# Optimization experiments

Hardware: AMD Instinct MI355X
Metric: run time of the kernel (lower is better)

Reference implementation:

```python
import jax, jax.numpy as jnp
import numpy as np
from jax import lax

DN = ('NHWC', 'HWIO', 'NHWC')


def _conv(x, w, b=None, stride=1):
    y = lax.conv_general_dilated(x, w, (stride, stride), 'SAME', dimension_numbers=DN)
    return y + b if b is not None else y


def _conv_t(x, w, b, stride=2):
    y = lax.conv_transpose(x, w, (stride, stride), 'SAME', dimension_numbers=DN)
    return y + b


def _res_stack(x, blocks):
    # ResidualBlock: x + Conv1x1(relu(Conv3x3(relu(x)))); final relu after stack
    for w1, w2 in blocks:
        t = jax.nn.relu(x)
        t = _conv(t, w1)          # 3x3, no bias
        t = jax.nn.relu(t)
        t = _conv(t, w2)          # 1x1, no bias
        x = x + t
    return jax.nn.relu(x)


def setup_inputs() -> dict:
    key = jax.random.key(0)
    ks = jax.random.split(key, 32)
    s = 0.05
    n = lambda i, shape: jax.random.normal(ks[i], shape, dtype=jnp.float32) * s
    H, RH, D, K = 128, 32, 128, 512
    return {
        'x': jax.random.normal(ks[0], (16, 256, 256, 3), dtype=jnp.float32),
        'emb': jax.random.normal(ks[1], (K, D), dtype=jnp.float32),  # stddev 1.0 init
        'enc_w1': n(2, (4, 4, 3, H // 2)),  'enc_b1': jnp.zeros((H // 2,), jnp.float32),
        'enc_w2': n(3, (4, 4, H // 2, H)),  'enc_b2': jnp.zeros((H,), jnp.float32),
        'enc_w3': n(4, (3, 3, H, H)),       'enc_b3': jnp.zeros((H,), jnp.float32),
        'erb1_w1': n(5, (3, 3, H, RH)), 'erb1_w2': n(6, (1, 1, RH, H)),
        'erb2_w1': n(7, (3, 3, H, RH)), 'erb2_w2': n(8, (1, 1, RH, H)),
        'dec_w': n(9, (3, 3, D, H)),        'dec_b': jnp.zeros((H,), jnp.float32),
        'drb1_w1': n(10, (3, 3, H, RH)), 'drb1_w2': n(11, (1, 1, RH, H)),
        'drb2_w1': n(12, (3, 3, H, RH)), 'drb2_w2': n(13, (1, 1, RH, H)),
        'dt1_w': n(14, (4, 4, H, H // 2)),  'dt1_b': jnp.zeros((H // 2,), jnp.float32),
        'dt2_w': n(15, (4, 4, H // 2, 3)),  'dt2_b': jnp.zeros((3,), jnp.float32),
    }


def _forward(x, emb, enc_w1, enc_b1, enc_w2, enc_b2, enc_w3, enc_b3,
             erb1_w1, erb1_w2, erb2_w1, erb2_w2,
             dec_w, dec_b, drb1_w1, drb1_w2, drb2_w1, drb2_w2,
             dt1_w, dt1_b, dt2_w, dt2_b):
    f = jax.nn.relu(_conv(x, enc_w1, enc_b1, 2))
    f = jax.nn.relu(_conv(f, enc_w2, enc_b2, 2))
    f = _conv(f, enc_w3, enc_b3, 1)
    f = _res_stack(f, [(erb1_w1, erb1_w2), (erb2_w1, erb2_w2)])
    # VQ: full [N, K] squared-distance matrix, argmin, codebook gather
    D = emb.shape[1]
    flat = f.reshape(-1, D)                                   # [N, D]
    dist = ((flat ** 2).sum(axis=1, keepdims=True)
            + (emb ** 2).sum(axis=1)[None, :]
            - 2.0 * flat @ emb.T)                              # [N, K]
    idx = jnp.argmin(dist, axis=1)                             # [N]
    q = emb[idx].reshape(f.shape)                              # quantized
    y = _conv(q, dec_w, dec_b, 1)
    y = _res_stack(y, [(drb1_w1, drb1_w2), (drb2_w1, drb2_w2)])
    y = jax.nn.relu(_conv_t(y, dt1_w, dt1_b))
    y = _conv_t(y, dt2_w, dt2_b)
    return (y, f, q)


def reference(x, emb, enc_w1, enc_b1, enc_w2, enc_b2, enc_w3, enc_b3,
              erb1_w1, erb1_w2, erb2_w1, erb2_w2,
              dec_w, dec_b, drb1_w1, drb1_w2, drb2_w1, drb2_w2,
              dt1_w, dt1_b, dt2_w, dt2_b):
    return _forward(x, emb, enc_w1, enc_b1, enc_w2, enc_b2, enc_w3, enc_b3,
                    erb1_w1, erb1_w2, erb2_w1, erb2_w2,
                    dec_w, dec_b, drb1_w1, drb1_w2, drb2_w1, drb2_w2,
                    dt1_w, dt1_b, dt2_w, dt2_b)
```

## Files before the change

### kernel.cpp

```cpp
#include <hip/hip_runtime.h>
#include <hip/hip_bf16.h>
#include <hip/hip_fp16.h>

using bf16 = __hip_bfloat16;
using frag_ab = __attribute__((ext_vector_type(8))) short;
using f16x8  = __attribute__((ext_vector_type(8))) _Float16;
using frag_cd = __attribute__((ext_vector_type(4))) float;

enum { F_INRELU = 1, F_OUTRELU = 2, F_RES = 4 };

struct TapSet { int dy[16]; int dx[16]; int wi[16]; };

__device__ __forceinline__ unsigned int relu_pk(unsigned int v) {
    unsigned int m = ((v & 0x80008000u) >> 15) * 0xFFFFu;
    return v & ~m;
}
__device__ __forceinline__ unsigned int mask_by(unsigned int v, unsigned int h) {
    unsigned int m = ((h & 0x80008000u) >> 15) * 0xFFFFu;
    return v & ~m;
}
__device__ __forceinline__ int xcd_swz(int bx, int n) {
    return (bx & 7) * (n >> 3) + (bx >> 3);
}

__global__ void pack_w_k(const float* __restrict__ w, bf16* __restrict__ dst,
                         int Ci, int Co, int BN, TapSet taps, int total)
{
    int idx = blockIdx.x * 256 + threadIdx.x;
    if (idx >= total) return;
    int j  = idx & 7;
    int r1 = idx >> 3;
    int nl = r1 % BN;
    int r2 = r1 / BN;
    int q  = r2 & 3;
    int cb = r2 >> 2;
    int nblocks = Co / BN;
    int c  = cb / nblocks;
    int nb = cb - c * nblocks;
    int cpt = Ci >> 5;
    int tap = c / cpt;
    int ci  = (c - tap * cpt) * 32 + q * 8 + j;
    int n   = nb * BN + nl;
    dst[idx] = __float2bfloat16(w[(size_t)(taps.wi[tap] * Ci + ci) * Co + n]);
}

__global__ void pack_w2_k(const float* __restrict__ w, __half* __restrict__ dst,
                          int Ci, int Co, int BN, TapSet taps, int total)
{
    int idx = blockIdx.x * 256 + threadIdx.x;
    if (idx >= total) return;
    int j  = idx & 7;
    int r1 = idx >> 3;
    int nl = r1 % BN;
    int r2 = r1 / BN;
    int q  = r2 & 3;
    int cb = r2 >> 2;
    int nblocks = Co / BN;
    int c  = cb / nblocks;
    int nb = cb - c * nblocks;
    int cpt = Ci >> 5;
    int tap = c / cpt;
    int ci  = (c - tap * cpt) * 32 + q * 8 + j;
    int n   = nb * BN + nl;
    float v = w[(size_t)(taps.wi[tap] * Ci + ci) * Co + n];
    __half h = __float2half(v);
    __half l = __float2half((v - __half2float(h)) * 2048.0f);
    size_t base = (size_t)cb * (BN * 64) + (q * BN + nl) * 8 + j;
    dst[base] = h;
    dst[base + BN * 32] = l;
}

__global__ void pack_wdt2_k(const float* __restrict__ w, __half* __restrict__ dst)
{
    int idx = blockIdx.x * 256 + threadIdx.x;
    if (idx >= 16384) return;
    int parity = idx >> 12;
    int r0 = idx & 4095;
    int j  = r0 & 7;
    int r1 = r0 >> 3;
    int nl = r1 & 15;
    int r2 = r1 >> 4;
    int q  = r2 & 3;
    int cb = r2 >> 2;
    int tap = cb >> 1;
    int cc  = cb & 1;
    int ci  = cc * 32 + q * 8 + j;
    int n   = nl;
    int py = parity >> 1, px = parity & 1;
    int ty = tap >> 1, tx = tap & 1;
    int wi = (py + 2 * ty) * 4 + (px + 2 * tx);
    float v = (n < 3) ? w[(size_t)(wi * 64 + ci) * 3 + n] : 0.f;
    __half h = __float2half(v);
    __half l = __float2half((v - __half2float(h)) * 2048.0f);
    size_t base = (size_t)parity * 8192 + cb * 1024 + (q * 16 + nl) * 8 + j;
    dst[base] = h;
    dst[base + 512] = l;
}

__global__ void pack_we1_k(const float* __restrict__ w, __half* __restrict__ dst)
{
    int idx = blockIdx.x * 256 + threadIdx.x;
    if (idx >= 4096) return;
    int j  = idx & 7;
    int r1 = idx >> 3;
    int nl = r1 & 63;
    int r2 = r1 >> 6;
    int q  = r2 & 3;
    int c  = r2 >> 2;
    int k  = c * 32 + q * 8 + j;
    int tap = k >> 2, ci = k & 3;
    float v = (ci < 3) ? w[(size_t)(tap * 3 + ci) * 64 + nl] : 0.f;
    __half h = __float2half(v);
    __half l = __float2half((v - __half2float(h)) * 2048.0f);
    size_t base = (size_t)c * 4096 + (q * 64 + nl) * 8 + j;
    dst[base] = h;
    dst[base + 2048] = l;
}

__global__ __launch_bounds__(256) void pad_x_k(
    const float* __restrict__ x, __half* __restrict__ xh, __half* __restrict__ xl)
{
    int pix = blockIdx.x * 256 + threadIdx.x;
    const float* ip = x + (size_t)pix * 3;
    float v0 = ip[0], v1 = ip[1], v2 = ip[2];
    unsigned short hb[4], lb[4];
    float vv[4] = {v0, v1, v2, 0.f};
#pragma unroll
    for (int i = 0; i < 4; ++i) {
        __half h = __float2half(vv[i]);
        hb[i] = __half_as_ushort(h);
        lb[i] = __half_as_ushort(__float2half((vv[i] - __half2float(h)) * 2048.0f));
    }
    uint2 hv = make_uint2((unsigned)hb[0] | ((unsigned)hb[1] << 16),
                          (unsigned)hb[2] | ((unsigned)hb[3] << 16));
    uint2 lv = make_uint2((unsigned)lb[0] | ((unsigned)lb[1] << 16),
                          (unsigned)lb[2] | ((unsigned)lb[3] << 16));
    *(uint2*)(xh + (size_t)pix * 4) = hv;
    *(uint2*)(xl + (size_t)pix * 4) = lv;
}

__global__ __launch_bounds__(256) void enc1_mfma_k(
    const __half* __restrict__ xh, const __half* __restrict__ xl,
    const __half* __restrict__ wp, const float* __restrict__ bias,
    __half* __restrict__ oh, __half* __restrict__ ol)
{
    __shared__ __align__(16) short Ash[64 * 32];
    __shared__ __align__(16) short Asl[64 * 32];
    __shared__ __align__(16) short Bsh[64 * 32];
    __shared__ __align__(16) short Bsl[64 * 32];

    const int tid = threadIdx.x;
    const int m0 = xcd_swz(blockIdx.x, 4096) * 64;

    const int am = tid >> 2;
    const int aq = tid & 3;
    const int gm  = m0 + am;
    const int nn_ = gm >> 14;
    const int rr_ = gm & 16383;
    const int iy0 = (rr_ >> 7) * 2 - 1;
    const int ix0 = (rr_ & 127) * 2 - 1;

    const int lane = tid & 63;
    const int wv4 = tid >> 6;
    const int wm = (wv4 & 1) * 32;
    const int wn = (wv4 >> 1) * 32;
    const int lm = lane & 15, lq = lane >> 4;

    frag_cd accA[2][2], accB[2][2];
#pragma unroll
    for (int i = 0; i < 2; ++i)
#pragma unroll
        for (int j = 0; j < 2; ++j)
#pragma unroll
            for (int r = 0; r < 4; ++r) { accA[i][j][r] = 0.f; accB[i][j][r] = 0.f; }

#pragma unroll
    for (int c = 0; c < 2; ++c) {
        const int tap = c * 8 + aq * 2;
        const int ky = tap >> 2, kx = tap & 3;
        const int iy = iy0 + ky;
        const int ix = ix0 + kx;
        uint2 h0 = make_uint2(0u, 0u), h1 = h0, l0 = h0, l1 = h0;
        if (iy >= 0 && iy < 256) {
            const size_t rowb = (size_t)(nn_ * 256 + iy) * 256;
            if (ix >= 0 && ix < 256) {
                h0 = *(const uint2*)(xh + (rowb + ix) * 4);
                l0 = *(const uint2*)(xl + (rowb + ix) * 4);
            }
            if (ix + 1 >= 0 && ix + 1 < 256) {
                h1 = *(const uint2*)(xh + (rowb + ix + 1) * 4);
                l1 = *(const uint2*)(xl + (rowb + ix + 1) * 4);
            }
        }
        __syncthreads();
        *(uint4*)&Ash[(aq * 64 + am) * 8] = make_uint4(h0.x, h0.y, h1.x, h1.y);
        *(uint4*)&Asl[(aq * 64 + am) * 8] = make_uint4(l0.x, l0.y, l1.x, l1.y);
        {
            const __half* wc = wp + (size_t)c * 4096;
            *(uint4*)&Bsh[tid * 8] = *(const uint4*)(wc + tid * 8);
            *(uint4*)&Bsl[tid * 8] = *(const uint4*)(wc + 2048 + tid * 8);
        }
        __syncthreads();

        f16x8 afh[2], afl[2], bfh[2], bfl[2];
#pragma unroll
        for (int i = 0; i < 2; ++i) {
            afh[i] = *(const f16x8*)&Ash[(lq * 64 + wm + i * 16 + lm) * 8];
            afl[i] = *(const f16x8*)&Asl[(lq * 64 + wm + i * 16 + lm) * 8];
        }
#pragma unroll
        for (int j = 0; j < 2; ++j) {
            bfh[j] = *(const f16x8*)&Bsh[(lq * 64 + wn + j * 16 + lm) * 8];
            bfl[j] = *(const f16x8*)&Bsl[(lq * 64 + wn + j * 16 + lm) * 8];
        }
#pragma unroll
        for (int i = 0; i < 2; ++i)
#pragma unroll
            for (int j = 0; j < 2; ++j) {
                accA[i][j] = __builtin_amdgcn_mfma_f32_16x16x32_f16(afh[i], bfh[j], accA[i][j], 0, 0, 0);
                accB[i][j] = __builtin_amdgcn_mfma_f32_16x16x32_f16(afh[i], bfl[j], accB[i][j], 0, 0, 0);
                accB[i][j] = __builtin_amdgcn_mfma_f32_16x16x32_f16(afl[i], bfh[j], accB[i][j], 0, 0, 0);
            }
    }

    const float s = 1.0f / 2048.0f;
#pragma unroll
    for (int j = 0; j < 2; ++j) {
        const int n_g = wn + j * 16 + lm;
        const float bv = bias[n_g];
#pragma unroll
        for (int i = 0; i < 2; ++i) {
#pragma unroll
            for (int r = 0; r < 4; ++r) {
                const int m_g = m0 + wm + i * 16 + lq * 4 + r;
                const size_t ob = (size_t)m_g * 64 + n_g;
                float v = accA[i][j][r] + accB[i][j][r] * s + bv;
                v = fmaxf(v, 0.f);
                __half h = __float2half(v);
                oh[ob] = h;
                ol[ob] = __float2half((v - __half2float(h)) * 2048.0f);
            }
        }
    }
}

template<int BN>
__global__ __launch_bounds__(256) void conv_mfma2_k(
    const __half* __restrict__ ah, const __half* __restrict__ al,
    const __half* __restrict__ wp, const float* __restrict__ bias,
    float* __restrict__ out, __half* __restrict__ oh, __half* __restrict__ ol,
    const __half* __restrict__ rh, const __half* __restrict__ rl,
    int IH, int IW, int Ci, int Co, int sy_in,
    TapSet taps, int ntaps, int flags)
{
    __shared__ __align__(16) short Ash[64 * 32];
    __shared__ __align__(16) short Asl[64 * 32];
    __shared__ __align__(16) short Bsh[BN * 32];
    __shared__ __align__(16) short Bsl[BN * 32];

    const int tid = threadIdx.x;
    const int m0 = xcd_swz(blockIdx.x, gridDim.x) * 64;
    const int n0 = blockIdx.y * BN;

    const int am = tid >> 2;
    const int aq = tid & 3;
    const int gm  = m0 + am;
    const int nn_ = gm >> 12;
    const int rr_ = gm & 4095;
    const int oy_ = (rr_ >> 6) * sy_in;
    const int ox_ = (rr_ & 63) * sy_in;

    const int lane = tid & 63;
    const int wv4 = tid >> 6;
    constexpr int MT = (BN >= 64) ? 2 : 1;
    constexpr int NT = (BN == 128) ? 4 : 2;
    const int wm = (BN >= 64) ? (wv4 & 1) * 32 : wv4 * 16;
    const int wn = (BN == 128) ? (wv4 >> 1) * 64 : ((BN == 64) ? (wv4 >> 1) * 32 : 0);
    const int lm = lane & 15, lq = lane >> 4;
    constexpr int NLOAD = BN * 32 / 8;

    frag_cd accA[MT][NT], accB[MT][NT];
#pragma unroll
    for (int i = 0; i < MT; ++i)
#pragma unroll
        for (int j = 0; j < NT; ++j)
#pragma unroll
            for (int r = 0; r < 4; ++r) { accA[i][j][r] = 0.f; accB[i][j][r] = 0.f; }

    const int cpt = Ci >> 5;
    const int nch = ntaps * cpt;
    const bool inrelu = (flags & F_INRELU) != 0;

    int tap = 0, cc = 0, ci0 = 0;
    for (int c = 0; c < nch; ++c) {
        const int iy = oy_ + taps.dy[tap];
        const int ix = ox_ + taps.dx[tap];
        uint4 avh = make_uint4(0u, 0u, 0u, 0u);
        uint4 avl = make_uint4(0u, 0u, 0u, 0u);
        if (iy >= 0 && iy < IH && ix >= 0 && ix < IW) {
            const size_t off = (size_t)((nn_ * IH + iy) * IW + ix) * Ci + ci0 + aq * 8;
            avh = *(const uint4*)(ah + off);
            avl = *(const uint4*)(al + off);
        }
        if (inrelu) {
            avl.x = mask_by(avl.x, avh.x); avl.y = mask_by(avl.y, avh.y);
            avl.z = mask_by(avl.z, avh.z); avl.w = mask_by(avl.w, avh.w);
            avh.x = relu_pk(avh.x); avh.y = relu_pk(avh.y);
            avh.z = relu_pk(avh.z); avh.w = relu_pk(avh.w);
        }
        uint4 bvh0, bvl0, bvh1, bvl1;
        {
            const __half* wc = wp + (size_t)(c * gridDim.y + blockIdx.y) * (BN * 64);
            if constexpr (BN == 128) {
                bvh0 = *(const uint4*)(wc + tid * 8);
                bvh1 = *(const uint4*)(wc + (256 + tid) * 8);
                bvl0 = *(const uint4*)(wc + BN * 32 + tid * 8);
                bvl1 = *(const uint4*)(wc + BN * 32 + (256 + tid) * 8);
            } else if (tid < NLOAD) {
                bvh0 = *(const uint4*)(wc + tid * 8);
                bvl0 = *(const uint4*)(wc + BN * 32 + tid * 8);
            }
        }

        __syncthreads();
        *(uint4*)&Ash[(aq * 64 + am) * 8] = avh;
        *(uint4*)&Asl[(aq * 64 + am) * 8] = avl;
        if constexpr (BN == 128) {
            *(uint4*)&Bsh[tid * 8] = bvh0;
            *(uint4*)&Bsh[(256 + tid) * 8] = bvh1;
            *(uint4*)&Bsl[tid * 8] = bvl0;
            *(uint4*)&Bsl[(256 + tid) * 8] = bvl1;
        } else if (tid < NLOAD) {
            *(uint4*)&Bsh[tid * 8] = bvh0;
            *(uint4*)&Bsl[tid * 8] = bvl0;
        }
        __syncthreads();

        f16x8 afh[MT], afl[MT], bfh[NT], bfl[NT];
#pragma unroll
        for (int i = 0; i < MT; ++i) {
            afh[i] = *(const f16x8*)&Ash[(lq * 64 + wm + i * 16 + lm) * 8];
            afl[i] = *(const f16x8*)&Asl[(lq * 64 + wm + i * 16 + lm) * 8];
        }
#pragma unroll
        for (int j = 0; j < NT; ++j) {
            bfh[j] = *(const f16x8*)&Bsh[(lq * BN + wn + j * 16 + lm) * 8];
            bfl[j] = *(const f16x8*)&Bsl[(lq * BN + wn + j * 16 + lm) * 8];
        }
#pragma unroll
        for (int i = 0; i < MT; ++i)
#pragma unroll
            for (int j = 0; j < NT; ++j) {
                accA[i][j] = __builtin_amdgcn_mfma_f32_16x16x32_f16(afh[i], bfh[j], accA[i][j], 0, 0, 0);
                accB[i][j] = __builtin_amdgcn_mfma_f32_16x16x32_f16(afh[i], bfl[j], accB[i][j], 0, 0, 0);
                accB[i][j] = __builtin_amdgcn_mfma_f32_16x16x32_f16(afl[i], bfh[j], accB[i][j], 0, 0, 0);
            }

        ci0 += 32;
        if (++cc == cpt) { cc = 0; ci0 = 0; ++tap; }
    }

    const float s = 1.0f / 2048.0f;
#pragma unroll
    for (int j = 0; j < NT; ++j) {
        const int n_g = n0 + wn + j * 16 + lm;
        const float bv = bias ? bias[n_g] : 0.f;
#pragma unroll
        for (int i = 0; i < MT; ++i) {
#pragma unroll
            for (int r = 0; r < 4; ++r) {
                const int m_g = m0 + wm + i * 16 + lq * 4 + r;
                const size_t ob = (size_t)m_g * Co + n_g;
                float v = accA[i][j][r] + accB[i][j][r] * s + bv;
                if (flags & F_RES)
                    v += __half2float(rh[ob]) + __half2float(rl[ob]) * s;
                if (flags & F_OUTRELU) v = fmaxf(v, 0.f);
                if (out) out[ob] = v;
                if (oh) {
                    __half h = __float2half(v);
                    oh[ob] = h;
                    ol[ob] = __float2half((v - __half2float(h)) * 2048.0f);
                }
            }
        }
    }
}

template<int BN>
__global__ __launch_bounds__(256) void conv_mfma_k(
    const bf16* __restrict__ a, const bf16* __restrict__ wp,
    const float* __restrict__ bias,
    float* __restrict__ out, bf16* __restrict__ out_bf,
    const float* __restrict__ res,
    int Ci, int Co, int OHf, int OWf, int sy_out, int py, int px,
    TapSet taps, int ntaps, int flags)
{
    __shared__ __align__(16) short As[64 * 32];
    __shared__ __align__(16) short Bs[BN * 32];

    const int tid = threadIdx.x;
    const int m0 = xcd_swz(blockIdx.x, gridDim.x) * 64;
    const int n0 = blockIdx.y * BN;

    const int am = tid >> 2;
    const int aq = tid & 3;
    const int gm  = m0 + am;
    const int nn_ = gm >> 12;
    const int rr_ = gm & 4095;
    const int oy_ = rr_ >> 6;
    const int ox_ = rr_ & 63;

    const int lane = tid & 63;
    const int wv4 = tid >> 6;
    constexpr int MT = (BN >= 64) ? 2 : 1;
    constexpr int NT = (BN == 128) ? 4 : 2;
    const int wm = (BN >= 64) ? (wv4 & 1) * 32 : wv4 * 16;
    const int wn = (BN == 128) ? (wv4 >> 1) * 64 : ((BN == 64) ? (wv4 >> 1) * 32 : 0);
    const int lm = lane & 15, lq = lane >> 4;
    constexpr int NLOAD = BN * 32 / 8;

    frag_cd acc[MT][NT];
#pragma unroll
    for (int i = 0; i < MT; ++i)
#pragma unroll
        for (int j = 0; j < NT; ++j)
#pragma unroll
            for (int r = 0; r < 4; ++r) acc[i][j][r] = 0.f;

    const int cpt = Ci >> 5;
    const int nch = ntaps * cpt;
    const bool inrelu = (flags & F_INRELU) != 0;

    int tap = 0, cc = 0, ci0 = 0;
    for (int c = 0; c < nch; ++c) {
        const int iy = oy_ + taps.dy[tap];
        const int ix = ox_ + taps.dx[tap];
        uint4 av = make_uint4(0u, 0u, 0u, 0u);
        if (iy >= 0 && iy < 64 && ix >= 0 && ix < 64)
            av = *(const uint4*)(a + (size_t)((nn_ * 64 + iy) * 64 + ix) * Ci + ci0 + aq * 8);
        if (inrelu) {
            av.x = relu_pk(av.x); av.y = relu_pk(av.y);
            av.z = relu_pk(av.z); av.w = relu_pk(av.w);
        }
        uint4 bv0, bv1;
        {
            const bf16* wc = wp + ((size_t)c * gridDim.y + blockIdx.y) * (BN * 32);
            if constexpr (BN == 128) {
                bv0 = *(const uint4*)(wc + tid * 8);
                bv1 = *(const uint4*)(wc + (256 + tid) * 8);
            } else if (tid < NLOAD) {
                bv0 = *(const uint4*)(wc + tid * 8);
            }
        }

        __syncthreads();
        *(uint4*)&As[(aq * 64 + am) * 8] = av;
        if constexpr (BN == 128) {
            *(uint4*)&Bs[tid * 8] = bv0;
            *(uint4*)&Bs[(256 + tid) * 8] = bv1;
        } else if (tid < NLOAD) {
            *(uint4*)&Bs[tid * 8] = bv0;
        }
        __syncthreads();

        frag_ab af[MT], bfr[NT];
#pragma unroll
        for (int i = 0; i < MT; ++i)
            af[i] = *(const frag_ab*)&As[(lq * 64 + wm + i * 16 + lm) * 8];
#pragma unroll
        for (int j = 0; j < NT; ++j)
            bfr[j] = *(const frag_ab*)&Bs[(lq * BN + wn + j * 16 + lm) * 8];
#pragma unroll
        for (int i = 0; i < MT; ++i)
#pragma unroll
            for (int j = 0; j < NT; ++j)
                acc[i][j] = __builtin_amdgcn_mfma_f32_16x16x32_bf16(af[i], bfr[j], acc[i][j], 0, 0, 0);

        ci0 += 32;
        if (++cc == cpt) { cc = 0; ci0 = 0; ++tap; }
    }

#pragma unroll
    for (int j = 0; j < NT; ++j) {
        const int n_g = n0 + wn + j * 16 + lm;
        const float bv = bias ? bias[n_g] : 0.f;
#pragma unroll
        for (int i = 0; i < MT; ++i) {
#pragma unroll
            for (int r = 0; r < 4; ++r) {
                const int m_g = m0 + wm + i * 16 + lq * 4 + r;
                const int nn2 = m_g >> 12;
                const int rr2 = m_g & 4095;
                const int oy = (rr2 >> 6) * sy_out + py;
                const int ox = (rr2 & 63) * sy_out + px;
                const size_t ob = ((size_t)(nn2 * OHf + oy) * OWf + ox) * Co + n_g;
                float v = acc[i][j][r] + bv;
                if (flags & F_RES)     v += res[ob];
                if (flags & F_OUTRELU) v = fmaxf(v, 0.f);
                if (out)    out[ob]    = v;
                if (out_bf) out_bf[ob] = __float2bfloat16(v);
            }
        }
    }
}

__global__ __launch_bounds__(256) void dt2_mfma_k(
    const float* __restrict__ in,
    const __half* __restrict__ wp,
    const float* __restrict__ bias,
    float* __restrict__ out)
{
    __shared__ __align__(16) short Ash[64 * 32];
    __shared__ __align__(16) short Asl[64 * 32];
    __shared__ __align__(16) short Bsh[16 * 32];
    __shared__ __align__(16) short Bsl[16 * 32];

    const int tid = threadIdx.x;
    const int bx  = xcd_swz(blockIdx.x, 16384);
    const int par = bx & 3;
    const int m0  = (bx >> 2) * 64;
    const int py = par >> 1, px = par & 1;

    const int am = tid >> 2;
    const int aq = tid & 3;
    const int gm  = m0 + am;
    const int nn_ = gm >> 14;
    const int rr_ = gm & 16383;
    const int r_  = rr_ >> 7;
    const int c_  = rr_ & 127;

    const int lane = tid & 63;
    const int wv4 = tid >> 6;
    const int wm = wv4 * 16;
    const int lm = lane & 15, lq = lane >> 4;

    frag_cd accA, accB;
#pragma unroll
    for (int r = 0; r < 4; ++r) { accA[r] = 0.f; accB[r] = 0.f; }

    const __half* wpar = wp + (size_t)par * 8192;

    for (int c = 0; c < 8; ++c) {
        const int tap = c >> 1;
        const int iy = r_ + py + (tap >> 1) - 1;
        const int ix = c_ + px + (tap & 1) - 1;
        const int ci0 = (c & 1) * 32;
        uint4 hi = make_uint4(0u, 0u, 0u, 0u);
        uint4 lo = make_uint4(0u, 0u, 0u, 0u);
        if ((unsigned)iy < 128u && (unsigned)ix < 128u) {
            const float* ip = in + (size_t)((nn_ * 128 + iy) * 128 + ix) * 64 + ci0 + aq * 8;
            const float4 v0 = *(const float4*)ip;
            const float4 v1 = *(const float4*)(ip + 4);
            float vv[8] = {v0.x, v0.y, v0.z, v0.w, v1.x, v1.y, v1.z, v1.w};
            unsigned short hb[8], lb[8];
#pragma unroll
            for (int i = 0; i < 8; ++i) {
                __half h = __float2half(vv[i]);
                hb[i] = __half_as_ushort(h);
                lb[i] = __half_as_ushort(__float2half((vv[i] - __half2float(h)) * 2048.0f));
            }
            hi = make_uint4((unsigned)hb[0] | ((unsigned)hb[1] << 16),
                            (unsigned)hb[2] | ((unsigned)hb[3] << 16),
                            (unsigned)hb[4] | ((unsigned)hb[5] << 16),
                            (unsigned)hb[6] | ((unsigned)hb[7] << 16));
            lo = make_uint4((unsigned)lb[0] | ((unsigned)lb[1] << 16),
                            (unsigned)lb[2] | ((unsigned)lb[3] << 16),
                            (unsigned)lb[4] | ((unsigned)lb[5] << 16),
                            (unsigned)lb[6] | ((unsigned)lb[7] << 16));
        }
        uint4 bvh, bvl;
        if (tid < 64) {
            const __half* wc = wpar + c * 1024;
            bvh = *(const uint4*)(wc + tid * 8);
            bvl = *(const uint4*)(wc + 512 + tid * 8);
        }

        __syncthreads();
        *(uint4*)&Ash[(aq * 64 + am) * 8] = hi;
        *(uint4*)&Asl[(aq * 64 + am) * 8] = lo;
        if (tid < 64) {
            *(uint4*)&Bsh[tid * 8] = bvh;
            *(uint4*)&Bsl[tid * 8] = bvl;
        }
        __syncthreads();

        const f16x8 afh = *(const f16x8*)&Ash[(lq * 64 + wm + lm) * 8];
        const f16x8 afl = *(const f16x8*)&Asl[(lq * 64 + wm + lm) * 8];
        const f16x8 bfh = *(const f16x8*)&Bsh[(lq * 16 + lm) * 8];
        const f16x8 bfl = *(const f16x8*)&Bsl[(lq * 16 + lm) * 8];
        accA = __builtin_amdgcn_mfma_f32_16x16x32_f16(afh, bfh, accA, 0, 0, 0);
        accB = __builtin_amdgcn_mfma_f32_16x16x32_f16(afh, bfl, accB, 0, 0, 0);
        accB = __builtin_amdgcn_mfma_f32_16x16x32_f16(afl, bfh, accB, 0, 0, 0);
    }

    const float s = 1.0f / 2048.0f;
    if (lm < 3) {
        const float bv = bias[lm];
#pragma unroll
        for (int r = 0; r < 4; ++r) {
            const int m_g = m0 + wm + lq * 4 + r;
            const int nn2 = m_g >> 14;
            const int rr2 = m_g & 16383;
            const int oy = (rr2 >> 7) * 2 + py;
            const int ox = (rr2 & 127) * 2 + px;
            out[((size_t)(nn2 * 256 + oy) * 256 + ox) * 3 + lm] = accA[r] + accB[r] * s + bv;
        }
    }
}

__global__ void enorm_k(const float* __restrict__ emb, float* __restrict__ en) {
    int k = blockIdx.x * 256 + threadIdx.x;
    if (k >= 512) return;
    const float4* e = (const float4*)(emb + k * 128);
    float s = 0.f;
    for (int i = 0; i < 32; ++i) {
        float4 v = e[i];
        s += v.x * v.x + v.y * v.y + v.z * v.z + v.w * v.w;
    }
    en[k] = s;
}

__global__ void pack_emb_k(const float* __restrict__ emb, __half* __restrict__ dst)
{
    int idx = blockIdx.x * 256 + threadIdx.x;
    int k = idx & 127;
    int n = idx >> 7;
    float v = emb[idx];
    __half h = __float2half(v);
    __half l = __float2half((v - __half2float(h)) * 2048.0f);
    int nb = n >> 6, nl = n & 63;
    int ch = k >> 5, q = (k >> 3) & 3, j = k & 7;
    size_t base = (size_t)(nb * 4 + ch) * 4096 + (q * 64 + nl) * 8 + j;
    dst[base] = h;
    dst[base + 2048] = l;
}

__global__ __launch_bounds__(256) void vq_mfma_k(
    const __half* __restrict__ fh, const __half* __restrict__ fl,
    const __half* __restrict__ pe, const float* __restrict__ en,
    const float* __restrict__ emb, float* __restrict__ q, bf16* __restrict__ qb)
{
    __shared__ __align__(16) short Ash[64 * 128];
    __shared__ __align__(16) short Asl[64 * 128];
    __shared__ int sel[64];

    const int tid  = threadIdx.x;
    const int pos0 = blockIdx.x * 64;

    {
        const int am = tid >> 2;
        const int aq = tid & 3;
#pragma unroll
        for (int ch = 0; ch < 4; ++ch) {
            const size_t off = (size_t)(pos0 + am) * 128 + ch * 32 + aq * 8;
            uint4 vh = *(const uint4*)(fh + off);
            uint4 vl = *(const uint4*)(fl + off);
            *(uint4*)&Ash[((ch * 4 + aq) * 64 + am) * 8] = vh;
            *(uint4*)&Asl[((ch * 4 + aq) * 64 + am) * 8] = vl;
        }
    }
    __syncthreads();

    const int lane = tid & 63;
    const int w    = tid >> 6;
    const int lm = lane & 15, lq = lane >> 4;
    const int mbase = w * 16;
    const float s = 1.0f / 2048.0f;

    float best[4] = {3.4e38f, 3.4e38f, 3.4e38f, 3.4e38f};
    int   bidx[4] = {0, 0, 0, 0};

    f16x8 ah[4], alv[4];
#pragma unroll
    for (int ch = 0; ch < 4; ++ch) {
        ah[ch]  = *(const f16x8*)&Ash[((ch * 4 + lq) * 64 + mbase + lm) * 8];
        alv[ch] = *(const f16x8*)&Asl[((ch * 4 + lq) * 64 + mbase + lm) * 8];
    }

    for (int nb = 0; nb < 8; ++nb) {
        frag_cd accA[4], accB[4];
#pragma unroll
        for (int j = 0; j < 4; ++j)
#pragma unroll
            for (int r = 0; r < 4; ++r) { accA[j][r] = 0.f; accB[j][r] = 0.f; }

#pragma unroll
        for (int ch = 0; ch < 4; ++ch) {
            const __half* base = pe + (size_t)(nb * 4 + ch) * 4096;
            f16x8 bh[4], bl[4];
#pragma unroll
            for (int j = 0; j < 4; ++j) {
                const int o = (lq * 64 + j * 16 + lm) * 8;
                bh[j] = *(const f16x8*)(base + o);
                bl[j] = *(const f16x8*)(base + 2048 + o);
            }
#pragma unroll
            for (int j = 0; j < 4; ++j) {
                accA[j] = __builtin_amdgcn_mfma_f32_16x16x32_f16(ah[ch], bh[j], accA[j], 0, 0, 0);
                accB[j] = __builtin_amdgcn_mfma_f32_16x16x32_f16(ah[ch], bl[j], accB[j], 0, 0, 0);
                accB[j] = __builtin_amdgcn_mfma_f32_16x16x32_f16(alv[ch], bh[j], accB[j], 0, 0, 0);
            }
        }

#pragma unroll
        for (int j = 0; j < 4; ++j) {
            const int code = nb * 64 + j * 16 + lm;
            const float ec = en[code];
#pragma unroll
            for (int r = 0; r < 4; ++r) {
                float dot = accA[j][r] + accB[j][r] * s;
                float d = fmaf(dot, -2.f, ec);
                if (d < best[r]) { best[r] = d; bidx[r] = code; }
            }
        }
    }

#pragma unroll
    for (int r = 0; r < 4; ++r) {
        float d = best[r]; int ix = bidx[r];
#pragma unroll
        for (int m = 1; m < 16; m <<= 1) {
            float d2 = __shfl_xor(d, m);
            int   x2 = __shfl_xor(ix, m);
            if (d2 < d || (d2 == d && x2 < ix)) { d = d2; ix = x2; }
        }
        if (lm == 0) sel[mbase + lq * 4 + r] = ix;
    }
    __syncthreads();

#pragma unroll
    for (int jj = 0; jj < 32; ++jj) {
        int id = jj * 256 + tid;
        int p = id >> 7, k = id & 127;
        float v = emb[(size_t)sel[p] * 128 + k];
        q[(size_t)(pos0 + p) * 128 + k]  = v;
        qb[(size_t)(pos0 + p) * 128 + k] = __float2bfloat16(v);
    }
}

static TapSet conv_taps(int KH, int KW, int pad) {
    TapSet t{};
    for (int ky = 0; ky < KH; ++ky)
        for (int kx = 0; kx < KW; ++kx) {
            int i = ky * KW + kx;
            t.dy[i] = ky - pad; t.dx[i] = kx - pad; t.wi[i] = i;
        }
    return t;
}

static TapSet convt_taps(int py, int px) {
    TapSet t{};
    for (int ty = 0; ty < 2; ++ty)
        for (int tx = 0; tx < 2; ++tx) {
            int i = ty * 2 + tx;
            t.dy[i] = py + ty - 1;
            t.dx[i] = px + tx - 1;
            t.wi[i] = (py + 2 * ty) * 4 + (px + 2 * tx);
        }
    return t;
}

extern "C" void kernel_launch(void* const* d_in, const int* in_sizes, int n_in,
                              void* d_out, int out_size, void* d_ws, size_t ws_size,
                              hipStream_t stream)
{
    const float* x       = (const float*)d_in[0];
    const float* emb     = (const float*)d_in[1];
    const float* enc_w1  = (const float*)d_in[2];
    const float* enc_b1  = (const float*)d_in[3];
    const float* enc_w2  = (const float*)d_in[4];
    const float* enc_b2  = (const float*)d_in[5];
    const float* enc_w3  = (const float*)d_in[6];
    const float* enc_b3  = (const float*)d_in[7];
    const float* erb1_w1 = (const float*)d_in[8];
    const float* erb1_w2 = (const float*)d_in[9];
    const float* erb2_w1 = (const float*)d_in[10];
    const float* erb2_w2 = (const float*)d_in[11];
    const float* dec_w   = (const float*)d_in[12];
    const float* dec_b   = (const float*)d_in[13];
    const float* drb1_w1 = (const float*)d_in[14];
    const float* drb1_w2 = (const float*)d_in[15];
    const float* drb2_w1 = (const float*)d_in[16];
    const float* drb2_w2 = (const float*)d_in[17];
    const float* dt1_w   = (const float*)d_in[18];
    const float* dt1_b   = (const float*)d_in[19];
    const float* dt2_w   = (const float*)d_in[20];
    const float* dt2_b   = (const float*)d_in[21];

    char* wsb = (char*)d_ws;
    __half* H1 = (__half*)wsb;
    __half* L1 = (__half*)(wsb + (size_t)33554432);
    __half* H2 = (__half*)(wsb + (size_t)67108864);
    __half* L2 = (__half*)(wsb + (size_t)83886080);
    __half* Xh = (__half*)(wsb + (size_t)67108864);
    __half* Xl = (__half*)(wsb + (size_t)75497472);
    __half* H3 = (__half*)wsb;
    __half* L3 = (__half*)(wsb + (size_t)16777216);
    __half* H4 = (__half*)(wsb + (size_t)33554432);
    __half* L4 = (__half*)(wsb + (size_t)50331648);
    __half* Ht = (__half*)(wsb + (size_t)100663296);
    __half* Lt = (__half*)(wsb + (size_t)104857600);
    float*  EN = (float*)(wsb + (size_t)109051904);
    __half* Fh = (__half*)wsb;
    __half* Fl = (__half*)(wsb + (size_t)16777216);
    bf16* Qb  = (bf16*)(wsb + (size_t)67108864);
    bf16* Db  = (bf16*)(wsb + (size_t)83886080);
    bf16* Y1b = Qb;
    bf16* Y2b = Db;
    bf16* Tb  = (bf16*)(wsb + (size_t)100663296);
    float* Y0 = (float*)wsb;
    float* Y1 = (float*)(wsb + (size_t)33554432);
    float* A1 = (float*)wsb;
    char* pk = wsb + (size_t)109056000;
    bf16* Pdec  = (bf16*)pk;  pk += 147456 * 2;
    bf16* Pd1w1 = (bf16*)pk;  pk += 36864 * 2;
    bf16* Pd1w2 = (bf16*)pk;  pk += 4096 * 2;
    bf16* Pd2w1 = (bf16*)pk;  pk += 36864 * 2;
    bf16* Pd2w2 = (bf16*)pk;  pk += 4096 * 2;
    bf16* Pdt1[4];
    for (int i = 0; i < 4; ++i) { Pdt1[i] = (bf16*)pk; pk += 65536 * 2; }
    __half* P2enc2 = (__half*)pk; pk += 131072 * 4;
    __half* P2enc3 = (__half*)pk; pk += 147456 * 4;
    __half* P2e1w1 = (__half*)pk; pk += 36864 * 4;
    __half* P2e1w2 = (__half*)pk; pk += 4096 * 4;
    __half* P2e2w1 = (__half*)pk; pk += 36864 * 4;
    __half* P2e2w2 = (__half*)pk; pk += 4096 * 4;
    __half* Pe     = (__half*)pk; pk += 131072 * 2;
    __half* Pe1    = (__half*)pk; pk += 8192 * 2;
    __half* Pdt2   = (__half*)pk; pk += 32768 * 2;

    float* outY = (float*)d_out;
    float* outF = outY + 3145728;
    float* outQ = outF + 8388608;

    const TapSet t3 = conv_taps(3, 3, 1);
    const TapSet t4 = conv_taps(4, 4, 1);
    const TapSet t1 = conv_taps(1, 1, 0);
    TapSet tdt[4];
    for (int p = 0; p < 4; ++p) tdt[p] = convt_taps(p >> 1, p & 1);

    enorm_k<<<2, 256, 0, stream>>>(emb, EN);
    pack_emb_k<<<256, 256, 0, stream>>>(emb, Pe);
    pack_we1_k<<<16, 256, 0, stream>>>(enc_w1, Pe1);
    pack_wdt2_k<<<64, 256, 0, stream>>>(dt2_w, Pdt2);

    pack_w_k<<<(147456 + 255) / 256, 256, 0, stream>>>(dec_w, Pdec, 128, 128, 128, t3, 147456);
    pack_w_k<<<(36864 + 255) / 256, 256, 0, stream>>>(drb1_w1, Pd1w1, 128, 32, 32, t3, 36864);
    pack_w_k<<<(4096 + 255) / 256, 256, 0, stream>>>(drb1_w2, Pd1w2, 32, 128, 128, t1, 4096);
    pack_w_k<<<(36864 + 255) / 256, 256, 0, stream>>>(drb2_w1, Pd2w1, 128, 32, 32, t3, 36864);
    pack_w_k<<<(4096 + 255) / 256, 256, 0, stream>>>(drb2_w2, Pd2w2, 32, 128, 128, t1, 4096);
    for (int p = 0; p < 4; ++p)
        pack_w_k<<<(65536 + 255) / 256, 256, 0, stream>>>(dt1_w, Pdt1[p], 128, 64, 64, tdt[p], 65536);
    pack_w2_k<<<(131072 + 255) / 256, 256, 0, stream>>>(enc_w2, P2enc2, 64, 128, 128, t4, 131072);
    pack_w2_k<<<(147456 + 255) / 256, 256, 0, stream>>>(enc_w3, P2enc3, 128, 128, 128, t3, 147456);
    pack_w2_k<<<(36864 + 255) / 256, 256, 0, stream>>>(erb1_w1, P2e1w1, 128, 32, 32, t3, 36864);
    pack_w2_k<<<(4096 + 255) / 256, 256, 0, stream>>>(erb1_w2, P2e1w2, 32, 128, 128, t1, 4096);
    pack_w2_k<<<(36864 + 255) / 256, 256, 0, stream>>>(erb2_w1, P2e2w1, 128, 32, 32, t3, 36864);
    pack_w2_k<<<(4096 + 255) / 256, 256, 0, stream>>>(erb2_w2, P2e2w2, 32, 128, 128, t1, 4096);

    pad_x_k<<<4096, 256, 0, stream>>>(x, Xh, Xl);
    enc1_mfma_k<<<4096, 256, 0, stream>>>(Xh, Xl, Pe1, enc_b1, H1, L1);
    conv_mfma2_k<128><<<dim3(1024, 1), 256, 0, stream>>>(H1, L1, P2enc2, enc_b2,
        nullptr, H2, L2, nullptr, nullptr, 128, 128, 64, 128, 2, t4, 16, F_OUTRELU);
    conv_mfma2_k<128><<<dim3(1024, 1), 256, 0, stream>>>(H2, L2, P2enc3, enc_b3,
        nullptr, H3, L3, nullptr, nullptr, 64, 64, 128, 128, 1, t3, 9, 0);
    conv_mfma2_k<32><<<dim3(1024, 1), 256, 0, stream>>>(H3, L3, P2e1w1, nullptr,
        nullptr, Ht, Lt, nullptr, nullptr, 64, 64, 128, 32, 1, t3, 9, F_INRELU);
    conv_mfma2_k<128><<<dim3(1024, 1), 256, 0, stream>>>(Ht, Lt, P2e1w2, nullptr,
        nullptr, H4, L4, H3, L3, 64, 64, 32, 128, 1, t1, 1, F_INRELU | F_RES);
    conv_mfma2_k<32><<<dim3(1024, 1), 256, 0, stream>>>(H4, L4, P2e2w1, nullptr,
        nullptr, Ht, Lt, nullptr, nullptr, 64, 64, 128, 32, 1, t3, 9, F_INRELU);
    conv_mfma2_k<128><<<dim3(1024, 1), 256, 0, stream>>>(Ht, Lt, P2e2w2, nullptr,
        outF, Fh, Fl, H4, L4, 64, 64, 32, 128, 1, t1, 1, F_INRELU | F_RES | F_OUTRELU);

    vq_mfma_k<<<1024, 256, 0, stream>>>(Fh, Fl, Pe, EN, emb, outQ, Qb);

    conv_mfma_k<128><<<dim3(1024, 1), 256, 0, stream>>>(Qb, Pdec, dec_b, Y0, Db, nullptr,
        128, 128, 64, 64, 1, 0, 0, t3, 9, 0);
    conv_mfma_k<32><<<dim3(1024, 1), 256, 0, stream>>>(Db, Pd1w1, nullptr, nullptr, Tb, nullptr,
        128, 32, 64, 64, 1, 0, 0, t3, 9, F_INRELU);
    conv_mfma_k<128><<<dim3(1024, 1), 256, 0, stream>>>(Tb, Pd1w2, nullptr, Y1, Y1b, Y0,
        32, 128, 64, 64, 1, 0, 0, t1, 1, F_INRELU | F_RES);
    conv_mfma_k<32><<<dim3(1024, 1), 256, 0, stream>>>(Y1b, Pd2w1, nullptr, nullptr, Tb, nullptr,
        128, 32, 64, 64, 1, 0, 0, t3, 9, F_INRELU);
    conv_mfma_k<128><<<dim3(1024, 1), 256, 0, stream>>>(Tb, Pd2w2, nullptr, nullptr, Y2b, Y1,
        32, 128, 64, 64, 1, 0, 0, t1, 1, F_INRELU | F_RES | F_OUTRELU);
    for (int p = 0; p < 4; ++p)
        conv_mfma_k<64><<<dim3(1024, 1), 256, 0, stream>>>(Y2b, Pdt1[p], dt1_b, A1, nullptr, nullptr,
            128, 64, 128, 128, 2, p >> 1, p & 1, tdt[p], 4, F_OUTRELU);

    dt2_mfma_k<<<16384, 256, 0, stream>>>(A1, Pdt2, dt2_b, outY);
}
```

Measured before the change: 834.0 us.

## Load dt2 MFMA fragments directly into registers, dropping LDS staging and barriers

The final transposed-conv kernel no longer stages inputs and weights through shared memory. Each lane loads its own A-fragment straight from global memory, and all eight weight chunks are preloaded into registers before a fully unrolled loop. This removes two __syncthreads per iteration and the LDS round trip. The float-to-half hi/lo split now uses packed round-toward-zero conversion (cvt_pkrtz) instead of round-to-nearest, which slightly changes rounding and raises register pressure.

Result: slower. 925.1 us (+10.9%).

```diff
diff --git a/kernel.cpp b/kernel.cpp
--- a/kernel.cpp
+++ b/kernel.cpp
@@ -5,6 +5,7 @@
 using bf16 = __hip_bfloat16;
 using frag_ab = __attribute__((ext_vector_type(8))) short;
 using f16x8  = __attribute__((ext_vector_type(8))) _Float16;
+using hf16x2 = __attribute__((ext_vector_type(2))) __fp16;
 using frag_cd = __attribute__((ext_vector_type(4))) float;
 
 enum { F_INRELU = 1, F_OUTRELU = 2, F_RES = 4 };
@@ -510,87 +511,60 @@
     const float* __restrict__ bias,
     float* __restrict__ out)
 {
-    __shared__ __align__(16) short Ash[64 * 32];
-    __shared__ __align__(16) short Asl[64 * 32];
-    __shared__ __align__(16) short Bsh[16 * 32];
-    __shared__ __align__(16) short Bsl[16 * 32];
-
     const int tid = threadIdx.x;
     const int bx  = xcd_swz(blockIdx.x, 16384);
     const int par = bx & 3;
     const int m0  = (bx >> 2) * 64;
     const int py = par >> 1, px = par & 1;
 
-    const int am = tid >> 2;
-    const int aq = tid & 3;
-    const int gm  = m0 + am;
-    const int nn_ = gm >> 14;
-    const int rr_ = gm & 16383;
-    const int r_  = rr_ >> 7;
-    const int c_  = rr_ & 127;
-
     const int lane = tid & 63;
     const int wv4 = tid >> 6;
     const int wm = wv4 * 16;
     const int lm = lane & 15, lq = lane >> 4;
 
+    const int m_g = m0 + wm + lm;
+    const int nn_ = m_g >> 14;
+    const int rr_ = m_g & 16383;
+    const int r_  = rr_ >> 7;
+    const int c_  = rr_ & 127;
+
+    const __half* wpar = wp + (size_t)par * 8192;
+    f16x8 bh[8], bl[8];
+#pragma unroll
+    for (int c = 0; c < 8; ++c) {
+        const __half* wc = wpar + c * 1024 + (lq * 16 + lm) * 8;
+        bh[c] = *(const f16x8*)wc;
+        bl[c] = *(const f16x8*)(wc + 512);
+    }
+
     frag_cd accA, accB;
 #pragma unroll
     for (int r = 0; r < 4; ++r) { accA[r] = 0.f; accB[r] = 0.f; }
 
-    const __half* wpar = wp + (size_t)par * 8192;
-
+#pragma unroll
     for (int c = 0; c < 8; ++c) {
         const int tap = c >> 1;
         const int iy = r_ + py + (tap >> 1) - 1;
         const int ix = c_ + px + (tap & 1) - 1;
         const int ci0 = (c & 1) * 32;
-        uint4 hi = make_uint4(0u, 0u, 0u, 0u);
-        uint4 lo = make_uint4(0u, 0u, 0u, 0u);
+        float4 v0 = make_float4(0.f, 0.f, 0.f, 0.f), v1 = v0;
         if ((unsigned)iy < 128u && (unsigned)ix < 128u) {
-            const float* ip = in + (size_t)((nn_ * 128 + iy) * 128 + ix) * 64 + ci0 + aq * 8;
-            const float4 v0 = *(const float4*)ip;
-            const float4 v1 = *(const float4*)(ip + 4);
-            float vv[8] = {v0.x, v0.y, v0.z, v0.w, v1.x, v1.y, v1.z, v1.w};
-            unsigned short hb[8], lb[8];
-#pragma unroll
-            for (int i = 0; i < 8; ++i) {
-                __half h = __float2half(vv[i]);
-                hb[i] = __half_as_ushort(h);
-                lb[i] = __half_as_ushort(__float2half((vv[i] - __half2float(h)) * 2048.0f));
-            }
-            hi = make_uint4((unsigned)hb[0] | ((unsigned)hb[1] << 16),
-                            (unsigned)hb[2] | ((unsigned)hb[3] << 16),
-                            (unsigned)hb[4] | ((unsigned)hb[5] << 16),
-                            (unsigned)hb[6] | ((unsigned)hb[7] << 16));
-            lo = make_uint4((unsigned)lb[0] | ((unsigned)lb[1] << 16),
-                            (unsigned)lb[2] | ((unsigned)lb[3] << 16),
-                            (unsigned)lb[4] | ((unsigned)lb[5] << 16),
-                            (unsigned)lb[6] | ((unsigned)lb[7] << 16));
-        }
-        uint4 bvh, bvl;
-        if (tid < 64) {
-            const __half* wc = wpar + c * 1024;
-            bvh = *(const uint4*)(wc + tid * 8);
-            bvl = *(const uint4*)(wc + 512 + tid * 8);
-        }
-
-        __syncthreads();
-        *(uint4*)&Ash[(aq * 64 + am) * 8] = hi;
-        *(uint4*)&Asl[(aq * 64 + am) * 8] = lo;
-        if (tid < 64) {
-            *(uint4*)&Bsh[tid * 8] = bvh;
-            *(uint4*)&Bsl[tid * 8] = bvl;
-        }
-        __syncthreads();
-
-        const f16x8 afh = *(const f16x8*)&Ash[(lq * 64 + wm + lm) * 8];
-        const f16x8 afl = *(const f16x8*)&Asl[(lq * 64 + wm + lm) * 8];
-        const f16x8 bfh = *(const f16x8*)&Bsh[(lq * 16 + lm) * 8];
-        const f16x8 bfl = *(const f16x8*)&Bsl[(lq * 16 + lm) * 8];
-        accA = __builtin_amdgcn_mfma_f32_16x16x32_f16(afh, bfh, accA, 0, 0, 0);
-        accB = __builtin_amdgcn_mfma_f32_16x16x32_f16(afh, bfl, accB, 0, 0, 0);
-        accB = __builtin_amdgcn_mfma_f32_16x16x32_f16(afl, bfh, accB, 0, 0, 0);
+            const float* ip = in + (size_t)((nn_ * 128 + iy) * 128 + ix) * 64 + ci0 + lq * 8;
+            v0 = *(const float4*)ip;
+            v1 = *(const float4*)(ip + 4);
+        }
+        const float vv[8] = {v0.x, v0.y, v0.z, v0.w, v1.x, v1.y, v1.z, v1.w};
+        union { hf16x2 p[4]; f16x8 v; } uh, ul;
+#pragma unroll
+        for (int i = 0; i < 4; ++i) {
+            hf16x2 h = __builtin_amdgcn_cvt_pkrtz(vv[2 * i], vv[2 * i + 1]);
+            uh.p[i] = h;
+            ul.p[i] = __builtin_amdgcn_cvt_pkrtz((vv[2 * i]     - (float)h[0]) * 2048.f,
+                                                 (vv[2 * i + 1] - (float)h[1]) * 2048.f);
+        }
+        accA = __builtin_amdgcn_mfma_f32_16x16x32_f16(uh.v, bh[c], accA, 0, 0, 0);
+        accB = __builtin_amdgcn_mfma_f32_16x16x32_f16(uh.v, bl[c], accB, 0, 0, 0);
+        accB = __builtin_amdgcn_mfma_f32_16x16x32_f16(ul.v, bh[c], accB, 0, 0, 0);
     }
 
     const float s = 1.0f / 2048.0f;
@@ -598,9 +572,9 @@
         const float bv = bias[lm];
 #pragma unroll
         for (int r = 0; r < 4; ++r) {
-            const int m_g = m0 + wm + lq * 4 + r;
-            const int nn2 = m_g >> 14;
-            const int rr2 = m_g & 16383;
+            const int m2 = m0 + wm + lq * 4 + r;
+            const int nn2 = m2 >> 14;
+            const int rr2 = m2 & 16383;
             const int oy = (rr2 >> 7) * 2 + py;
             const int ox = (rr2 & 127) * 2 + px;
             out[((size_t)(nn2 * 256 + oy) * 256 + ox) * 3 + lm] = accA[r] + accB[r] * s + bv;
```
